# Performance work log

Measured on AMD Instinct MI355X. Metric: run time of the kernel, lower is better.

The kernel has to match this reference:

```python
import jax, jax.numpy as jnp
import numpy as np

NEG_SLOPE = 0.2

def _gat_layer(x, src, dst, W, a_src, a_dst, bias, concat):
    # x: [N, F_in]; W: [F_in, H*C]; a_src/a_dst: [H, C]; bias: [H*C] or [C]
    N = x.shape[0]
    H, C = a_src.shape
    h = (x @ W).reshape(N, H, C)                      # node features per head
    e_src = jnp.einsum('nhc,hc->nh', h, a_src)        # [N, H]
    e_dst = jnp.einsum('nhc,hc->nh', h, a_dst)        # [N, H]
    e = jax.nn.leaky_relu(e_src[src] + e_dst[dst], NEG_SLOPE)  # [E, H]
    # segment softmax over incoming edges of each destination node
    m = jax.ops.segment_max(e, dst, num_segments=N)   # [N, H]
    p = jnp.exp(e - m[dst])
    denom = jax.ops.segment_sum(p, dst, num_segments=N)
    alpha = p / denom[dst]                            # [E, H]
    msg = h[src] * alpha[:, :, None]                  # [E, H, C]
    out = jax.ops.segment_sum(msg, dst, num_segments=N)  # [N, H, C]
    if concat:
        out = out.reshape(N, H * C) + bias
    else:
        out = out.mean(axis=1) + bias
    return out, alpha


def setup_inputs() -> dict:
    key = jax.random.key(0)
    ks = jax.random.split(key, 12)
    N, E = 20000, 320000
    F_in, Ch, Co, H = 256, 64, 64, 8
    x = jax.random.normal(ks[0], (N, F_in), dtype=jnp.float32)
    edge_index = jax.random.randint(ks[1], (2, E), 0, N, dtype=jnp.int64)
    s = 0.05
    return {
        'x': x,
        'edge_index': edge_index,
        'W1': jax.random.normal(ks[2], (F_in, H * Ch), dtype=jnp.float32) * s,
        'att_src1': jax.random.normal(ks[3], (H, Ch), dtype=jnp.float32) * s,
        'att_dst1': jax.random.normal(ks[4], (H, Ch), dtype=jnp.float32) * s,
        'b1': jnp.zeros((H * Ch,), dtype=jnp.float32),
        'W2': jax.random.normal(ks[5], (H * Ch, H * Co), dtype=jnp.float32) * s,
        'att_src2': jax.random.normal(ks[6], (H, Co), dtype=jnp.float32) * s,
        'att_dst2': jax.random.normal(ks[7], (H, Co), dtype=jnp.float32) * s,
        'b2': jnp.zeros((Co,), dtype=jnp.float32),
    }


def reference(x, edge_index, W1, att_src1, att_dst1, b1, W2, att_src2, att_dst2, b2):
    N = x.shape[0]
    # PyG GATConv adds self-loops by default
    loop = jnp.arange(N, dtype=edge_index.dtype)
    src = jnp.concatenate([edge_index[0], loop])
    dst = jnp.concatenate([edge_index[1], loop])
    h1, alpha1 = _gat_layer(x, src, dst, W1, att_src1, att_dst1, b1, concat=True)
    h1 = jax.nn.relu(h1)
    h2, alpha2 = _gat_layer(h1, src, dst, W2, att_src2, att_dst2, b2, concat=False)
    return h2, alpha1, alpha2
```

## Files before the change

kernel.cpp:

```cpp
#include <hip/hip_runtime.h>

#define H 8
#define C 64
#define HC 512
#define NEG 0.2f

typedef __attribute__((ext_vector_type(8))) _Float16 half8v;
typedef __attribute__((ext_vector_type(4))) _Float16 half4v;
typedef __attribute__((ext_vector_type(4))) float f32x4;

__device__ __forceinline__ float leaky(float x) { return x > 0.f ? x : NEG * x; }

#define GLOAD_LDS16(gp, lp) \
  __builtin_amdgcn_global_load_lds((const __attribute__((address_space(1))) unsigned int*)(gp), \
                                   (__attribute__((address_space(3))) unsigned int*)(lp), 16, 0, 0)

__global__ void k_degree(const int* __restrict__ ei, int E, int N, int* __restrict__ deg) {
    int e = blockIdx.x * blockDim.x + threadIdx.x;
    int Et = E + N;
    if (e >= Et) return;
    int d = (e < E) ? ei[E + e] : (e - E);
    atomicAdd(&deg[d], 1);
}

__global__ __launch_bounds__(1024) void k_scan(const int* __restrict__ deg, int N, int* __restrict__ row_start) {
    __shared__ int part[1024];
    int t = threadIdx.x;
    int chunk = (N + 1023) >> 10;
    int lo = t * chunk, hi = min(lo + chunk, N);
    int s = 0;
    for (int i = lo; i < hi; ++i) s += deg[i];
    part[t] = s;
    __syncthreads();
    for (int off = 1; off < 1024; off <<= 1) {
        int v = (t >= off) ? part[t - off] : 0;
        __syncthreads();
        part[t] += v;
        __syncthreads();
    }
    int base = (t == 0) ? 0 : part[t - 1];
    for (int i = lo; i < hi; ++i) { row_start[i] = base; base += deg[i]; }
    if (t == 1023) row_start[N] = part[1023];
}

__global__ void k_fill(const int* __restrict__ ei, int E, int N,
                       const int* __restrict__ row_start, int* __restrict__ cursor,
                       int* __restrict__ csr_src, int* __restrict__ csr_eid) {
    int e = blockIdx.x * blockDim.x + threadIdx.x;
    int Et = E + N;
    if (e >= Et) return;
    int d, s;
    if (e < E) { s = ei[e]; d = ei[E + e]; } else { s = e - E; d = s; }
    int pos = atomicAdd(&cursor[d], 1);
    int idx = row_start[d] + pos;
    csr_src[idx] = s;
    csr_eid[idx] = e;
}

__global__ void k_tofp16(const float* __restrict__ in, _Float16* __restrict__ out, int n4) {
    int i = blockIdx.x * blockDim.x + threadIdx.x;
    if (i >= n4) return;
    float4 v = reinterpret_cast<const float4*>(in)[i];
    half4v h;
    h[0] = (_Float16)v.x; h[1] = (_Float16)v.y;
    h[2] = (_Float16)v.z; h[3] = (_Float16)v.w;
    reinterpret_cast<half4v*>(out)[i] = h;
}

__global__ void k_tsplit(const float* __restrict__ W, _Float16* __restrict__ th,
                         _Float16* __restrict__ tl, int K, int Nc) {
    int idx = blockIdx.x * blockDim.x + threadIdx.x;
    if (idx >= K * Nc) return;
    int c = idx / K, k = idx - c * K;
    float v = W[(long)k * Nc + c];
    _Float16 hh = (_Float16)v;
    th[idx] = hh;
    tl[idx] = (_Float16)(v - (float)hh);
}

__global__ __launch_bounds__(256) void k_gemm_mfma(const _Float16* __restrict__ A,
                                                   const _Float16* __restrict__ Bh,
                                                   const _Float16* __restrict__ Bl,
                                                   _Float16* __restrict__ Cc, int M, int K, int Pb,
                                                   const float* __restrict__ a_src, const float* __restrict__ a_dst,
                                                   float* __restrict__ e_src, float* __restrict__ e_dst) {
    __shared__ _Float16 lA[8192], lBh[8192], lBl[8192];
    int bid = blockIdx.x;
    int panel = ((bid >> 5) << 3) + (bid & 7);
    int colb  = (bid >> 3) & 3;
    if (panel >= Pb) return;
    int tid = threadIdx.x;
    int w = tid >> 6, lane = tid & 63;
    int wr = w >> 1, wc = w & 1;
    int r0 = panel * 128, c0 = colb * 128;
    f32x4 acc[4][4] = {};
    int frag_off = ((lane >> 4) * 16 + (lane & 15)) * 8;

    int rb0 = tid >> 6, kc0 = (tid >> 4) & 3, r16_0 = tid & 15;
    int rb1 = (256 + tid) >> 6, kc1 = ((256 + tid) >> 4) & 3;
    long gaBase0 = (long)(r0 + rb0 * 16 + r16_0) * K + kc0 * 8;
    long gbBase0 = (long)(c0 + rb0 * 16 + r16_0) * K + kc0 * 8;
    long gaBase1 = (long)(r0 + rb1 * 16 + r16_0) * K + kc1 * 8;
    long gbBase1 = (long)(c0 + rb1 * 16 + r16_0) * K + kc1 * 8;
    int ldst0 = (w * 64) * 8;
    int ldst1 = (256 + w * 64) * 8;

#define STAGE(buf, k0)  do { \
        int off = (buf) * 4096; \
        GLOAD_LDS16(A  + gaBase0 + (k0), lA  + off + ldst0); \
        GLOAD_LDS16(Bh + gbBase0 + (k0), lBh + off + ldst0); \
        GLOAD_LDS16(Bl + gbBase0 + (k0), lBl + off + ldst0); \
        GLOAD_LDS16(A  + gaBase1 + (k0), lA  + off + ldst1); \
        GLOAD_LDS16(Bh + gbBase1 + (k0), lBh + off + ldst1); \
        GLOAD_LDS16(Bl + gbBase1 + (k0), lBl + off + ldst1); \
    } while (0)

    int nk = K >> 5;
    STAGE(0, 0);
    __syncthreads();
    int cur = 0;
    for (int t = 0; t < nk; ++t) {
        if (t + 1 < nk) STAGE(cur ^ 1, (t + 1) * 32);
        int off = cur * 4096;
        half8v fa[4], fbh[4], fbl[4];
        #pragma unroll
        for (int m = 0; m < 4; ++m) {
            int sa = off + (wr * 4 + m) * 512 + frag_off;
            fa[m] = *reinterpret_cast<half8v*>(&lA[sa]);
            int sb = off + (wc * 4 + m) * 512 + frag_off;
            fbh[m] = *reinterpret_cast<half8v*>(&lBh[sb]);
            fbl[m] = *reinterpret_cast<half8v*>(&lBl[sb]);
        }
        #pragma unroll
        for (int m = 0; m < 4; ++m)
            #pragma unroll
            for (int n = 0; n < 4; ++n) {
                acc[m][n] = __builtin_amdgcn_mfma_f32_16x16x32_f16(fa[m], fbh[n], acc[m][n], 0, 0, 0);
                acc[m][n] = __builtin_amdgcn_mfma_f32_16x16x32_f16(fa[m], fbl[n], acc[m][n], 0, 0, 0);
            }
        __syncthreads();
        cur ^= 1;
    }
#undef STAGE

    int head = colb * 2 + wc;
    #pragma unroll
    for (int m = 0; m < 4; ++m)
        #pragma unroll
        for (int j = 0; j < 4; ++j) {
            int gr = r0 + wr * 64 + m * 16 + (lane >> 4) * 4 + j;
            if (gr < M) {
                #pragma unroll
                for (int n = 0; n < 4; ++n)
                    Cc[(long)gr * HC + head * 64 + n * 16 + (lane & 15)] = (_Float16)acc[m][n][j];
            }
        }
    float asv[4], adv[4];
    #pragma unroll
    for (int nn = 0; nn < 4; ++nn) {
        asv[nn] = a_src[head * 64 + nn * 16 + (lane & 15)];
        adv[nn] = a_dst[head * 64 + nn * 16 + (lane & 15)];
    }
    #pragma unroll
    for (int m = 0; m < 4; ++m)
        #pragma unroll
        for (int j = 0; j < 4; ++j) {
            int gr = r0 + wr * 64 + m * 16 + (lane >> 4) * 4 + j;
            float es = 0.f, ed = 0.f;
            #pragma unroll
            for (int nn = 0; nn < 4; ++nn) {
                es = fmaf(acc[m][nn][j], asv[nn], es);
                ed = fmaf(acc[m][nn][j], adv[nn], ed);
            }
            #pragma unroll
            for (int o = 1; o < 16; o <<= 1) {
                es += __shfl_xor(es, o);
                ed += __shfl_xor(ed, o);
            }
            if ((lane & 15) == 0 && gr < M) {
                e_src[gr * 8 + head] = es;
                e_dst[gr * 8 + head] = ed;
            }
        }
}

__global__ __launch_bounds__(512) void k_agg(const half8v* __restrict__ hp8,
                                             const float* __restrict__ e_src,
                                             const float* __restrict__ e_dst,
                                             const int* __restrict__ row_start,
                                             const int* __restrict__ csr_src,
                                             const int* __restrict__ csr_eid,
                                             const float* __restrict__ bias,
                                             float* __restrict__ h2out,
                                             _Float16* __restrict__ h1,
                                             float* __restrict__ alpha,
                                             int N, int concat) {
    __shared__ float pbuf[8][512];
    __shared__ int   sibuf[8][64];
    __shared__ int   eibuf[8][64];
    int wid = threadIdx.x >> 6, lane = threadIdx.x & 63;
    int n = blockIdx.x * 8 + wid;
    if (n >= N) return;
    int lo3 = lane & 7, hi3 = lane >> 3;
    int row = row_start[n];
    int deg = row_start[n + 1] - row;
    int chunks = (deg + 7) >> 3;
    bool small = (deg <= 64);
    float* pw = &pbuf[wid][0];
    float ed = e_dst[n * 8 + lo3];
    float psum = 0.f;
    int idx0 = row + min(lo3, deg - 1);
    int sraw = csr_src[idx0];
    int eidr = csr_eid[idx0];
    for (int c = 0; c < chunks; ++c) {
        int sraw_c = sraw, eidr_c = eidr;
        if (c + 1 < chunks) {
            int idxn = row + min((c + 1) * 8 + lo3, deg - 1);
            sraw = csr_src[idxn];
            eidr = csr_eid[idxn];
        }
        if (small) { sibuf[wid][c * 8 + lo3] = sraw_c; eibuf[wid][c * 8 + lo3] = eidr_c; }
        int sv = __shfl(sraw_c, hi3);
        float es = e_src[sv * 8 + lo3];
        float p = __expf(leaky(es + ed));
        if (c * 8 + hi3 >= deg) p = 0.f;
        psum += p;
        if (small) pw[c * 64 + lane] = p;
    }
    psum += __shfl_xor(psum, 8);
    psum += __shfl_xor(psum, 16);
    psum += __shfl_xor(psum, 32);
    float inv = 1.0f / psum;
    float acc[8] = {};
    for (int c = 0; c < chunks; ++c) {
        float p; int sraw_c, eidr_c;
        if (small) {
            sraw_c = sibuf[wid][c * 8 + lo3];
            eidr_c = eibuf[wid][c * 8 + lo3];
            p = pw[c * 64 + lane];
        } else {
            int idx = row + min(c * 8 + lo3, deg - 1);
            sraw_c = csr_src[idx];
            eidr_c = csr_eid[idx];
            int sv = __shfl(sraw_c, hi3);
            float es = e_src[sv * 8 + lo3];
            p = __expf(leaky(es + ed));
            if (c * 8 + hi3 >= deg) p = 0.f;
        }
        int eid = __shfl(eidr_c, hi3);
        if (c * 8 + hi3 < deg)
            alpha[(long)eid * 8 + lo3] = p * inv;
        #pragma unroll
        for (int eg = 0; eg < 8; ++eg) {
            float pe = __shfl(p, eg * 8 + hi3);
            int   se = __shfl(sraw_c, eg);
            half8v hv = hp8[(long)se * 64 + lane];
            #pragma unroll
            for (int k = 0; k < 8; ++k)
                acc[k] = fmaf((float)hv[k], pe, acc[k]);
        }
    }
    float invg = __shfl(inv, hi3);
    if (concat) {
        const float4* b4 = reinterpret_cast<const float4*>(bias);
        float4 ba = b4[lane * 2], bb = b4[lane * 2 + 1];
        float bv[8] = {ba.x, ba.y, ba.z, ba.w, bb.x, bb.y, bb.z, bb.w};
        half8v hh;
        #pragma unroll
        for (int k = 0; k < 8; ++k) {
            float v = fmaf(acc[k], invg, bv[k]);
            v = v > 0.f ? v : 0.f;
            hh[k] = (_Float16)v;
        }
        reinterpret_cast<half8v*>(h1)[(long)n * 64 + lane] = hh;
    } else {
        float sc = invg * 0.125f;
        #pragma unroll
        for (int k = 0; k < 8; ++k) acc[k] *= sc;
        #pragma unroll
        for (int o = 8; o <= 32; o <<= 1)
            #pragma unroll
            for (int k = 0; k < 8; ++k)
                acc[k] += __shfl_xor(acc[k], o);
        if (hi3 == 0) {
            float4 r0, r1;
            r0.x = acc[0] + bias[lo3 * 8 + 0];
            r0.y = acc[1] + bias[lo3 * 8 + 1];
            r0.z = acc[2] + bias[lo3 * 8 + 2];
            r0.w = acc[3] + bias[lo3 * 8 + 3];
            r1.x = acc[4] + bias[lo3 * 8 + 4];
            r1.y = acc[5] + bias[lo3 * 8 + 5];
            r1.z = acc[6] + bias[lo3 * 8 + 6];
            r1.w = acc[7] + bias[lo3 * 8 + 7];
            float4* o4 = reinterpret_cast<float4*>(h2out + (long)n * 64 + lo3 * 8);
            o4[0] = r0;
            o4[1] = r1;
        }
    }
}

extern "C" void kernel_launch(void* const* d_in, const int* in_sizes, int n_in,
                              void* d_out, int out_size, void* d_ws, size_t ws_size,
                              hipStream_t stream) {
    const float* x   = (const float*)d_in[0];
    const int*   ei  = (const int*)d_in[1];
    const float* W1  = (const float*)d_in[2];
    const float* as1 = (const float*)d_in[3];
    const float* ad1 = (const float*)d_in[4];
    const float* b1  = (const float*)d_in[5];
    const float* W2  = (const float*)d_in[6];
    const float* as2 = (const float*)d_in[7];
    const float* ad2 = (const float*)d_in[8];
    const float* b2  = (const float*)d_in[9];

    int N  = in_sizes[0] / 256;
    int E  = in_sizes[1] / 2;
    int Et = E + N;
    int K1 = 256;
    int Mb   = (N + 127) / 128;
    int Mpad = Mb * 128;

    float* out    = (float*)d_out;
    float* h2_out = out;
    float* alpha1 = out + (size_t)N * 64;
    float* alpha2 = alpha1 + (size_t)Et * H;

    _Float16* hpre = (_Float16*)d_ws;
    _Float16* h1   = hpre + (size_t)Mpad * HC;
    _Float16* xh   = h1 + (size_t)Mpad * HC;
    _Float16* W1th = xh + (size_t)Mpad * K1;
    _Float16* W1tl = W1th + (size_t)HC * K1;
    _Float16* W2th = W1tl + (size_t)HC * K1;
    _Float16* W2tl = W2th + (size_t)HC * HC;
    float* eS     = (float*)(W2tl + (size_t)HC * HC);
    float* eD     = eS + (size_t)N * H;
    int*   deg    = (int*)(eD + (size_t)N * H);
    int*   cursor = deg + N;
    int*   row_st = cursor + N;
    int*   csr_src= row_st + N + 1;
    int*   csr_eid= csr_src + Et;

    hipMemsetAsync(deg, 0, (size_t)2 * N * sizeof(int), stream);
    int tb = 256;
    k_degree<<<(Et + tb - 1) / tb, tb, 0, stream>>>(ei, E, N, deg);
    k_scan<<<1, 1024, 0, stream>>>(deg, N, row_st);
    k_fill<<<(Et + tb - 1) / tb, tb, 0, stream>>>(ei, E, N, row_st, cursor, csr_src, csr_eid);

    int n4 = N * K1 / 4;
    k_tofp16<<<(n4 + tb - 1) / tb, tb, 0, stream>>>(x, xh, n4);
    k_tsplit<<<(K1 * HC + tb - 1) / tb, tb, 0, stream>>>(W1, W1th, W1tl, K1, HC);
    k_tsplit<<<(HC * HC + tb - 1) / tb, tb, 0, stream>>>(W2, W2th, W2tl, HC, HC);

    int Pb8 = ((Mb + 7) / 8) * 8;
    int ggemm = Pb8 * 4;
    int gagg = (N + 7) / 8;
    k_gemm_mfma<<<ggemm, 256, 0, stream>>>(xh, W1th, W1tl, hpre, N, K1, Mb, as1, ad1, eS, eD);
    k_agg<<<gagg, 512, 0, stream>>>((const half8v*)hpre, eS, eD, row_st, csr_src, csr_eid,
                                    b1, nullptr, h1, alpha1, N, 1);
    k_gemm_mfma<<<ggemm, 256, 0, stream>>>(h1, W2th, W2tl, hpre, N, HC, Mb, as2, ad2, eS, eD);
    k_agg<<<gagg, 512, 0, stream>>>((const half8v*)hpre, eS, eD, row_st, csr_src, csr_eid,
                                    b2, h2_out, nullptr, alpha2, N, 0);
}
```

Measured before the change: 258.8 us.

## Split aggregation into edge-softmax and head-major gather kernels

The GEMM now writes projected features in a head-major layout ([H][Mpad][64]). The fused aggregation kernel is split into k_edge, which computes the softmax normaliser and alpha, and k_gather, which assigns one block per node group and head and reads only that head's 128-byte slice per source node. This is meant to improve cache locality of the random-source feature gathers by partitioning work by head. In exchange it recomputes the exponentials, adds extra launches, and adds an fp16 intermediate plus a separate mean kernel for layer 2. That intermediate adds rounding and memory traffic.

After: 342.8 us. +32.5%, slower.

```diff
diff --git a/kernel.cpp b/kernel.cpp
--- a/kernel.cpp
+++ b/kernel.cpp
@@ -81,7 +81,7 @@
 __global__ __launch_bounds__(256) void k_gemm_mfma(const _Float16* __restrict__ A,
                                                    const _Float16* __restrict__ Bh,
                                                    const _Float16* __restrict__ Bl,
-                                                   _Float16* __restrict__ Cc, int M, int K, int Pb,
+                                                   _Float16* __restrict__ Cc, int M, int K, int Pb, int Mpad,
                                                    const float* __restrict__ a_src, const float* __restrict__ a_dst,
                                                    float* __restrict__ e_src, float* __restrict__ e_dst) {
     __shared__ _Float16 lA[8192], lBh[8192], lBl[8192];
@@ -144,6 +144,7 @@
 #undef STAGE
 
     int head = colb * 2 + wc;
+    long hbase = (long)head * Mpad * 64;
     #pragma unroll
     for (int m = 0; m < 4; ++m)
         #pragma unroll
@@ -152,7 +153,7 @@
             if (gr < M) {
                 #pragma unroll
                 for (int n = 0; n < 4; ++n)
-                    Cc[(long)gr * HC + head * 64 + n * 16 + (lane & 15)] = (_Float16)acc[m][n][j];
+                    Cc[hbase + (long)gr * 64 + n * 16 + (lane & 15)] = (_Float16)acc[m][n][j];
             }
         }
     float asv[4], adv[4];
@@ -184,20 +185,15 @@
         }
 }
 
-__global__ __launch_bounds__(512) void k_agg(const half8v* __restrict__ hp8,
-                                             const float* __restrict__ e_src,
-                                             const float* __restrict__ e_dst,
-                                             const int* __restrict__ row_start,
-                                             const int* __restrict__ csr_src,
-                                             const int* __restrict__ csr_eid,
-                                             const float* __restrict__ bias,
-                                             float* __restrict__ h2out,
-                                             _Float16* __restrict__ h1,
-                                             float* __restrict__ alpha,
-                                             int N, int concat) {
+__global__ __launch_bounds__(512) void k_edge(const float* __restrict__ e_src,
+                                              const float* __restrict__ e_dst,
+                                              const int* __restrict__ row_start,
+                                              const int* __restrict__ csr_src,
+                                              const int* __restrict__ csr_eid,
+                                              float* __restrict__ inv_buf,
+                                              float* __restrict__ alpha,
+                                              int N) {
     __shared__ float pbuf[8][512];
-    __shared__ int   sibuf[8][64];
-    __shared__ int   eibuf[8][64];
     int wid = threadIdx.x >> 6, lane = threadIdx.x & 63;
     int n = blockIdx.x * 8 + wid;
     if (n >= N) return;
@@ -209,18 +205,10 @@
     float* pw = &pbuf[wid][0];
     float ed = e_dst[n * 8 + lo3];
     float psum = 0.f;
-    int idx0 = row + min(lo3, deg - 1);
-    int sraw = csr_src[idx0];
-    int eidr = csr_eid[idx0];
     for (int c = 0; c < chunks; ++c) {
-        int sraw_c = sraw, eidr_c = eidr;
-        if (c + 1 < chunks) {
-            int idxn = row + min((c + 1) * 8 + lo3, deg - 1);
-            sraw = csr_src[idxn];
-            eidr = csr_eid[idxn];
-        }
-        if (small) { sibuf[wid][c * 8 + lo3] = sraw_c; eibuf[wid][c * 8 + lo3] = eidr_c; }
-        int sv = __shfl(sraw_c, hi3);
+        int idx = row + min(c * 8 + lo3, deg - 1);
+        int sraw = csr_src[idx];
+        int sv = __shfl(sraw, hi3);
         float es = e_src[sv * 8 + lo3];
         float p = __expf(leaky(es + ed));
         if (c * 8 + hi3 >= deg) p = 0.f;
@@ -231,72 +219,108 @@
     psum += __shfl_xor(psum, 16);
     psum += __shfl_xor(psum, 32);
     float inv = 1.0f / psum;
-    float acc[8] = {};
+    if (hi3 == 0) inv_buf[n * 8 + lo3] = inv;
     for (int c = 0; c < chunks; ++c) {
-        float p; int sraw_c, eidr_c;
+        float p;
+        int idx = row + min(c * 8 + lo3, deg - 1);
         if (small) {
-            sraw_c = sibuf[wid][c * 8 + lo3];
-            eidr_c = eibuf[wid][c * 8 + lo3];
             p = pw[c * 64 + lane];
         } else {
-            int idx = row + min(c * 8 + lo3, deg - 1);
-            sraw_c = csr_src[idx];
-            eidr_c = csr_eid[idx];
-            int sv = __shfl(sraw_c, hi3);
+            int sraw = csr_src[idx];
+            int sv = __shfl(sraw, hi3);
             float es = e_src[sv * 8 + lo3];
             p = __expf(leaky(es + ed));
             if (c * 8 + hi3 >= deg) p = 0.f;
         }
-        int eid = __shfl(eidr_c, hi3);
+        int eidr = csr_eid[idx];
+        int eid = __shfl(eidr, hi3);
         if (c * 8 + hi3 < deg)
             alpha[(long)eid * 8 + lo3] = p * inv;
-        #pragma unroll
-        for (int eg = 0; eg < 8; ++eg) {
-            float pe = __shfl(p, eg * 8 + hi3);
-            int   se = __shfl(sraw_c, eg);
-            half8v hv = hp8[(long)se * 64 + lane];
-            #pragma unroll
-            for (int k = 0; k < 8; ++k)
-                acc[k] = fmaf((float)hv[k], pe, acc[k]);
-        }
-    }
-    float invg = __shfl(inv, hi3);
-    if (concat) {
-        const float4* b4 = reinterpret_cast<const float4*>(bias);
-        float4 ba = b4[lane * 2], bb = b4[lane * 2 + 1];
-        float bv[8] = {ba.x, ba.y, ba.z, ba.w, bb.x, bb.y, bb.z, bb.w};
-        half8v hh;
-        #pragma unroll
-        for (int k = 0; k < 8; ++k) {
-            float v = fmaf(acc[k], invg, bv[k]);
-            v = v > 0.f ? v : 0.f;
-            hh[k] = (_Float16)v;
-        }
-        reinterpret_cast<half8v*>(h1)[(long)n * 64 + lane] = hh;
-    } else {
-        float sc = invg * 0.125f;
-        #pragma unroll
-        for (int k = 0; k < 8; ++k) acc[k] *= sc;
-        #pragma unroll
-        for (int o = 8; o <= 32; o <<= 1)
-            #pragma unroll
-            for (int k = 0; k < 8; ++k)
-                acc[k] += __shfl_xor(acc[k], o);
-        if (hi3 == 0) {
-            float4 r0, r1;
-            r0.x = acc[0] + bias[lo3 * 8 + 0];
-            r0.y = acc[1] + bias[lo3 * 8 + 1];
-            r0.z = acc[2] + bias[lo3 * 8 + 2];
-            r0.w = acc[3] + bias[lo3 * 8 + 3];
-            r1.x = acc[4] + bias[lo3 * 8 + 4];
-            r1.y = acc[5] + bias[lo3 * 8 + 5];
-            r1.z = acc[6] + bias[lo3 * 8 + 6];
-            r1.w = acc[7] + bias[lo3 * 8 + 7];
-            float4* o4 = reinterpret_cast<float4*>(h2out + (long)n * 64 + lo3 * 8);
-            o4[0] = r0;
-            o4[1] = r1;
-        }
-    }
+    }
+}
+
+__global__ __launch_bounds__(512) void k_gather(const half8v* __restrict__ hp8,
+                                                const float* __restrict__ e_src,
+                                                const float* __restrict__ e_dst,
+                                                const int* __restrict__ row_start,
+                                                const int* __restrict__ csr_src,
+                                                const float* __restrict__ inv_buf,
+                                                const float* __restrict__ bias,
+                                                _Float16* __restrict__ h1,
+                                                _Float16* __restrict__ accq,
+                                                int N, int Mpad, int concat) {
+    int wid = threadIdx.x >> 6, lane = threadIdx.x & 63;
+    int bid = blockIdx.x;
+    int h = bid & 7;
+    int n = (bid >> 3) * 8 + wid;
+    if (n >= N) return;
+    int eg = lane >> 3, cg = lane & 7;
+    long hoff = (long)h * Mpad * 8;
+    int row = row_start[n];
+    int deg = row_start[n + 1] - row;
+    int chunks = (deg + 7) >> 3;
+    float ed = e_dst[n * 8 + h];
+    float acc[8] = {};
+    for (int c = 0; c < chunks; ++c) {
+        int e0 = c * 8 + eg;
+        int idx = row + min(e0, deg - 1);
+        int s = csr_src[idx];
+        float es = e_src[s * 8 + h];
+        float p = (e0 < deg) ? __expf(leaky(es + ed)) : 0.f;
+        half8v hv = hp8[hoff + (long)s * 8 + cg];
+        #pragma unroll
+        for (int k = 0; k < 8; ++k)
+            acc[k] = fmaf((float)hv[k], p, acc[k]);
+    }
+    #pragma unroll
+    for (int o = 8; o <= 32; o <<= 1)
+        #pragma unroll
+        for (int k = 0; k < 8; ++k)
+            acc[k] += __shfl_xor(acc[k], o);
+    float inv = inv_buf[n * 8 + h];
+    if (eg == 0) {
+        if (concat) {
+            half8v hh;
+            #pragma unroll
+            for (int k = 0; k < 8; ++k) {
+                float v = fmaf(acc[k], inv, bias[h * 64 + cg * 8 + k]);
+                v = v > 0.f ? v : 0.f;
+                hh[k] = (_Float16)v;
+            }
+            reinterpret_cast<half8v*>(h1)[(long)n * 64 + h * 8 + cg] = hh;
+        } else {
+            half8v hv2;
+            #pragma unroll
+            for (int k = 0; k < 8; ++k) hv2[k] = (_Float16)(acc[k] * inv);
+            reinterpret_cast<half8v*>(accq)[hoff + (long)n * 8 + cg] = hv2;
+        }
+    }
+}
+
+__global__ void k_mean(const _Float16* __restrict__ accq, const float* __restrict__ bias,
+                       float* __restrict__ out, int N, int Mpad) {
+    int i = blockIdx.x * blockDim.x + threadIdx.x;
+    if (i >= N * 8) return;
+    int n = i >> 3, cg = i & 7;
+    float s[8] = {};
+    #pragma unroll
+    for (int h = 0; h < 8; ++h) {
+        half8v v = reinterpret_cast<const half8v*>(accq)[(long)h * Mpad * 8 + (long)n * 8 + cg];
+        #pragma unroll
+        for (int k = 0; k < 8; ++k) s[k] += (float)v[k];
+    }
+    float4 r0, r1;
+    r0.x = s[0] * 0.125f + bias[cg * 8 + 0];
+    r0.y = s[1] * 0.125f + bias[cg * 8 + 1];
+    r0.z = s[2] * 0.125f + bias[cg * 8 + 2];
+    r0.w = s[3] * 0.125f + bias[cg * 8 + 3];
+    r1.x = s[4] * 0.125f + bias[cg * 8 + 4];
+    r1.y = s[5] * 0.125f + bias[cg * 8 + 5];
+    r1.z = s[6] * 0.125f + bias[cg * 8 + 6];
+    r1.w = s[7] * 0.125f + bias[cg * 8 + 7];
+    float4* o4 = reinterpret_cast<float4*>(out + (long)n * 64 + cg * 8);
+    o4[0] = r0;
+    o4[1] = r1;
 }
 
 extern "C" void kernel_launch(void* const* d_in, const int* in_sizes, int n_in,
@@ -327,14 +351,16 @@
 
     _Float16* hpre = (_Float16*)d_ws;
     _Float16* h1   = hpre + (size_t)Mpad * HC;
-    _Float16* xh   = h1 + (size_t)Mpad * HC;
+    _Float16* accq = h1 + (size_t)Mpad * HC;
+    _Float16* xh   = accq + (size_t)Mpad * HC;
     _Float16* W1th = xh + (size_t)Mpad * K1;
     _Float16* W1tl = W1th + (size_t)HC * K1;
     _Float16* W2th = W1tl + (size_t)HC * K1;
     _Float16* W2tl = W2th + (size_t)HC * HC;
     float* eS     = (float*)(W2tl + (size_t)HC * HC);
     float* eD     = eS + (size_t)N * H;
-    int*   deg    = (int*)(eD + (size_t)N * H);
+    float* invb   = eD + (size_t)N * H;
+    int*   deg    = (int*)(invb + (size_t)N * H);
     int*   cursor = deg + N;
     int*   row_st = cursor + N;
     int*   csr_src= row_st + N + 1;
@@ -353,11 +379,15 @@
 
     int Pb8 = ((Mb + 7) / 8) * 8;
     int ggemm = Pb8 * 4;
-    int gagg = (N + 7) / 8;
-    k_gemm_mfma<<<ggemm, 256, 0, stream>>>(xh, W1th, W1tl, hpre, N, K1, Mb, as1, ad1, eS, eD);
-    k_agg<<<gagg, 512, 0, stream>>>((const half8v*)hpre, eS, eD, row_st, csr_src, csr_eid,
-                                    b1, nullptr, h1, alpha1, N, 1);
-    k_gemm_mfma<<<ggemm, 256, 0, stream>>>(h1, W2th, W2tl, hpre, N, HC, Mb, as2, ad2, eS, eD);
-    k_agg<<<gagg, 512, 0, stream>>>((const half8v*)hpre, eS, eD, row_st, csr_src, csr_eid,
-                                    b2, h2_out, nullptr, alpha2, N, 0);
-}
+    int gedge = (N + 7) / 8;
+    int ggath = ((N + 7) / 8) * 8;
+    k_gemm_mfma<<<ggemm, 256, 0, stream>>>(xh, W1th, W1tl, hpre, N, K1, Mb, Mpad, as1, ad1, eS, eD);
+    k_edge<<<gedge, 512, 0, stream>>>(eS, eD, row_st, csr_src, csr_eid, invb, alpha1, N);
+    k_gather<<<ggath, 512, 0, stream>>>((const half8v*)hpre, eS, eD, row_st, csr_src, invb,
+                                        b1, h1, nullptr, N, Mpad, 1);
+    k_gemm_mfma<<<ggemm, 256, 0, stream>>>(h1, W2th, W2tl, hpre, N, HC, Mb, Mpad, as2, ad2, eS, eD);
+    k_edge<<<gedge, 512, 0, stream>>>(eS, eD, row_st, csr_src, csr_eid, invb, alpha2, N);
+    k_gather<<<ggath, 512, 0, stream>>>((const half8v*)hpre, eS, eD, row_st, csr_src, invb,
+                                        b2, nullptr, accq, N, Mpad, 0);
+    k_mean<<<(N * 8 + tb - 1) / tb, tb, 0, stream>>>(accq, b2, h2_out, N, Mpad);
+}
```
